# Performance work log

Hardware: AMD Instinct MI355X
Metric: run time of the kernel (lower is better)

The kernel has to match this reference:

```python
import jax, jax.numpy as jnp
import numpy as np

EPS = 1e-12
N_HEADS = 16


def _ln(x, g, b, eps=EPS):
    m = jnp.mean(x, axis=-1, keepdims=True)
    v = jnp.var(x, axis=-1, keepdims=True)
    return (x - m) * jax.lax.rsqrt(v + eps) * g + b


def setup_inputs() -> dict:
    key = jax.random.key(0)
    ks = jax.random.split(key, 8)
    B, S, D, I = 2, 2048, 1024, 4096
    s = 0.02
    f32 = jnp.float32
    return {
        "x": jax.random.normal(ks[0], (B, S, D), f32),
        "input_mask": jnp.zeros((B, 1, 1, S), f32),  # additive mask, 0 = no masking
        "norm_w": jnp.ones((D,), f32),
        "norm_b": jnp.zeros((D,), f32),
        "attn_qkvw": jax.random.normal(ks[1], (D, 3 * D), f32) * s,
        "attn_qkvb": jnp.zeros((3 * D,), f32),
        "attn_ow": jax.random.normal(ks[2], (D, D), f32) * s,
        "attn_ob": jnp.zeros((D,), f32),
        "attn_nw": jnp.ones((D,), f32),
        "attn_nb": jnp.zeros((D,), f32),
        "inter_w": jax.random.normal(ks[3], (D, I), f32) * s,
        "inter_b": jnp.zeros((I,), f32),
        "inter_w1": jax.random.normal(ks[4], (D, I), f32) * s,
        "output_w": jax.random.normal(ks[5], (I, D), f32) * s,
        "output_b": jnp.zeros((D,), f32),
    }


def reference(x, input_mask, norm_w, norm_b, attn_qkvw, attn_qkvb, attn_ow,
              attn_ob, attn_nw, attn_nb, inter_w, inter_b, inter_w1,
              output_w, output_b):
    B, S, D = x.shape
    hd = D // N_HEADS

    # --- fused qkv_gemm: pre-layernorm + QKV GEMM + bias ---
    ln1 = _ln(x, norm_w, norm_b)
    qkv = ln1 @ attn_qkvw + attn_qkvb            # [B,S,3D]
    q, k, v = jnp.split(qkv, 3, axis=-1)

    def to_heads(t):  # [B,S,D] -> [B,H,S,hd]
        return t.reshape(B, S, N_HEADS, hd).transpose(0, 2, 1, 3)

    q, k, v = to_heads(q), to_heads(k), to_heads(v)

    # --- softmax-context attention (scale_attention=True -> 1/sqrt(head_dim)) ---
    scores = jnp.einsum('bhqd,bhkd->bhqk', q, k) / jnp.sqrt(jnp.float32(hd))
    scores = scores + input_mask                 # additive mask [B,1,1,S]
    probs = jax.nn.softmax(scores, axis=-1)
    ctx = jnp.einsum('bhqk,bhkd->bhqd', probs, v)
    ctx = ctx.transpose(0, 2, 1, 3).reshape(B, S, D)

    attn_out = ctx @ attn_ow                     # vector_matmul (no bias)

    # --- fused mlp_gemm: bias+residual add, layernorm, GEMM+bias+gelu ---
    residual_add = attn_out + attn_ob + x
    ln2 = _ln(residual_add, attn_nw, attn_nb)
    intermediate = jax.nn.gelu(ln2 @ inter_w + inter_b, approximate=False)
    # gated path: vector_matmul(mlp input, inter_w1) * intermediate (per source)
    intermediate = (attn_out @ inter_w1) * intermediate

    # --- output projection + bias_residual ---
    out = intermediate @ output_w + output_b + residual_add
    return out
```

## Files before the change

kernel.cpp:

```cpp
#include <hip/hip_runtime.h>
#include <hip/hip_bf16.h>

#define BATCH 2
#define SEQ   2048
#define DIM   1024
#define IDIM  4096
#define NH    16
#define HD    64
#define TOK   (BATCH * SEQ)

typedef __hip_bfloat16 bf16;

typedef short bf16x8_t __attribute__((ext_vector_type(8)));
typedef float f32x4_t  __attribute__((ext_vector_type(4)));

__device__ __forceinline__ float ldv(const float* p, size_t i) { return p[i]; }
__device__ __forceinline__ float ldv(const bf16*  p, size_t i) { return __bfloat162float(p[i]); }
__device__ __forceinline__ void  stv(float* p, size_t i, float v) { p[i] = v; }
__device__ __forceinline__ void  stv(bf16*  p, size_t i, float v) { p[i] = __float2bfloat16(v); }

__device__ __forceinline__ f32x4_t mfma16(bf16x8_t a, bf16x8_t b, f32x4_t c) {
    return __builtin_amdgcn_mfma_f32_16x16x32_bf16(a, b, c, 0, 0, 0);
}

__device__ __forceinline__ void gload16(const bf16* g, bf16* l) {
    __builtin_amdgcn_global_load_lds(
        (const __attribute__((address_space(1))) void*)g,
        (__attribute__((address_space(3))) void*)l, 16, 0, 0);
}

__global__ __launch_bounds__(256) void ln_kernel(const float* __restrict__ in,
                                                 const float* __restrict__ w,
                                                 const float* __restrict__ b,
                                                 bf16* __restrict__ out) {
    const int row = blockIdx.x;
    const int tid = threadIdx.x;
    const float* xr = in + (size_t)row * DIM;

    float v[4], sum = 0.f, sq = 0.f;
#pragma unroll
    for (int i = 0; i < 4; i++) {
        float t = xr[tid + i * 256];
        v[i] = t; sum += t; sq += t * t;
    }
#pragma unroll
    for (int off = 32; off >= 1; off >>= 1) {
        sum += __shfl_xor(sum, off);
        sq  += __shfl_xor(sq,  off);
    }
    __shared__ float s1[4], s2[4];
    int wid = tid >> 6;
    if ((tid & 63) == 0) { s1[wid] = sum; s2[wid] = sq; }
    __syncthreads();
    sum = s1[0] + s1[1] + s1[2] + s1[3];
    sq  = s2[0] + s2[1] + s2[2] + s2[3];

    const float mean = sum * (1.f / DIM);
    const float var  = fmaxf(sq * (1.f / DIM) - mean * mean, 0.f);
    const float rstd = rsqrtf(var + 1e-12f);

    bf16* orow = out + (size_t)row * DIM;
#pragma unroll
    for (int i = 0; i < 4; i++) {
        int idx = tid + i * 256;
        orow[idx] = __float2bfloat16((v[i] - mean) * rstd * w[idx] + b[idx]);
    }
}

__global__ __launch_bounds__(256) void wconv_kernel(const float* __restrict__ W,
                                                    bf16* __restrict__ Wt,
                                                    int K, int N) {
    __shared__ float tile[32][33];
    const int tid = threadIdx.x;
    const int n0 = blockIdx.x * 32;
    const int k0 = blockIdx.y * 32;
    const int c = tid & 31;
    const int r = tid >> 5;
#pragma unroll
    for (int i = 0; i < 4; i++)
        tile[r + i * 8][c] = W[(size_t)(k0 + r + i * 8) * N + n0 + c];
    __syncthreads();
#pragma unroll
    for (int i = 0; i < 4; i++)
        Wt[(size_t)(n0 + r + i * 8) * K + k0 + c] = __float2bfloat16(tile[c][r + i * 8]);
}

#define GBK 32

template<typename TX, int MODE, int TM, int TN>
__global__ __launch_bounds__(256) void mgemm_kernel(const bf16* __restrict__ A,
                                                    const bf16* __restrict__ Bt,
                                                    const float* __restrict__ bias,
                                                    const TX* __restrict__ aux,
                                                    TX* __restrict__ C,
                                                    const float* __restrict__ bias2,
                                                    const float* __restrict__ xin,
                                                    float* __restrict__ C2,
                                                    int M, int N, int K) {
    constexpr int TILE_M = TM * 32;
    constexpr int TILE_N = TN * 32;
    __shared__ alignas(16) bf16 As[TILE_M][GBK];
    __shared__ alignas(16) bf16 Bs[TILE_N][GBK];

    const int tid  = threadIdx.x;
    const int w    = tid >> 6;
    const int lane = tid & 63;
    const int cl   = lane & 15;
    const int qd   = lane >> 4;
    const int wm   = w >> 1;
    const int wn   = w & 1;

    const int gn   = gridDim.x;
    const int lin  = blockIdx.y * gn + blockIdx.x;
    const int span = 8 * gn;
    const int panel = lin / span;
    const int rem   = lin - panel * span;
    const int by    = panel * 8 + (rem & 7);
    const int bx    = rem >> 3;

    const int row0 = by * TILE_M;
    const int col0 = bx * TILE_N;

    const int lrow = lane >> 2;
    const int lkg  = lane & 3;

    f32x4_t acc[TM][TN];
#pragma unroll
    for (int m = 0; m < TM; m++)
#pragma unroll
        for (int n = 0; n < TN; n++) acc[m][n] = {0.f, 0.f, 0.f, 0.f};

    for (int k0 = 0; k0 < K; k0 += GBK) {
        __syncthreads();
#pragma unroll
        for (int i = 0; i < TM / 2; i++) {
            const int r16 = (w * (TM / 2) + i) * 16;
            gload16(A + (size_t)(row0 + r16 + lrow) * K + k0 + lkg * 8, &As[r16][0]);
        }
#pragma unroll
        for (int j = 0; j < TN / 2; j++) {
            const int r16 = (w * (TN / 2) + j) * 16;
            gload16(Bt + (size_t)(col0 + r16 + lrow) * K + k0 + lkg * 8, &Bs[r16][0]);
        }
        __syncthreads();

        bf16x8_t af[TM], bfr[TN];
#pragma unroll
        for (int m = 0; m < TM; m++)
            af[m] = *(const bf16x8_t*)&As[wm * (TM * 16) + m * 16 + cl][qd * 8];
#pragma unroll
        for (int n = 0; n < TN; n++)
            bfr[n] = *(const bf16x8_t*)&Bs[wn * (TN * 16) + n * 16 + cl][qd * 8];
#pragma unroll
        for (int m = 0; m < TM; m++)
#pragma unroll
            for (int n = 0; n < TN; n++)
                acc[m][n] = mfma16(af[m], bfr[n], acc[m][n]);
    }

#pragma unroll
    for (int m = 0; m < TM; m++) {
#pragma unroll
        for (int n = 0; n < TN; n++) {
            const int gc = col0 + wn * (TN * 16) + n * 16 + cl;
            const float bv = (MODE != 2 && MODE != 4 && bias) ? bias[gc] : 0.f;
#pragma unroll
            for (int r = 0; r < 4; r++) {
                const int gr = row0 + wm * (TM * 16) + m * 16 + qd * 4 + r;
                float c = acc[m][n][r] + bv;
                if (MODE == 1) {
                    c = 0.5f * c * (1.f + erff(c * 0.70710678118654752f));
                } else if (MODE == 2) {
                    c *= ldv(aux, (size_t)gr * N + gc);
                } else if (MODE == 3) {
                    c += ldv(aux, (size_t)gr * N + gc);
                }
                stv(C, (size_t)gr * N + gc, c);
                if (MODE == 4) {
                    C2[(size_t)gr * N + gc] = c + bias2[gc] + xin[(size_t)gr * N + gc];
                }
            }
        }
    }
}

#define KCH 64
#define LDP 72
#define NCH (SEQ / KCH)

__global__ __launch_bounds__(256) void attn_mfma_kernel(const bf16* __restrict__ qkv,
                                                        const float* __restrict__ mask,
                                                        bf16* __restrict__ ctx) {
    __shared__ alignas(16) bf16 Klds[KCH][LDP];
    __shared__ alignas(16) bf16 Vtlds[HD][LDP];
    __shared__ alignas(16) bf16 P2[4][4][4][4][16];

    const int tid  = threadIdx.x;
    const int w    = tid >> 6;
    const int lane = tid & 63;
    const int cl   = lane & 15;
    const int qd   = lane >> 4;

    const int qtile = blockIdx.x;
    const int bh    = blockIdx.y;
    const int bb    = bh >> 4;
    const int h     = bh & 15;

    const bf16*  base = qkv + (size_t)bb * SEQ * (3 * DIM) + h * HD;
    const float* mrow = mask + (size_t)bb * SEQ;

    const bf16* qrow = base + (size_t)(qtile * 64 + w * 16 + cl) * (3 * DIM);
    const bf16x8_t aq0 = *(const bf16x8_t*)(qrow + qd * 8);
    const bf16x8_t aq1 = *(const bf16x8_t*)(qrow + 32 + qd * 8);

    const bf16x8_t onesv = {0x3F80, 0x3F80, 0x3F80, 0x3F80,
                            0x3F80, 0x3F80, 0x3F80, 0x3F80};

    const int krow0 = tid >> 3;
    const int kcol  = (tid & 7) * 8;

    bf16x8_t kx[2], vx[2];
    float    mvx[4];
#pragma unroll
    for (int i = 0; i < 2; i++)
        kx[i] = *(const bf16x8_t*)(base + (size_t)(krow0 + i * 32) * (3 * DIM) + DIM + kcol);
#pragma unroll
    for (int p = 0; p < 2; p++)
        vx[p] = *(const bf16x8_t*)(base + (size_t)lane * (3 * DIM) + 2 * DIM + (w + p * 4) * 8);
#pragma unroll
    for (int ks = 0; ks < 4; ks++) mvx[ks] = mrow[ks * 16 + cl];

    f32x4_t O[4] = {{0,0,0,0},{0,0,0,0},{0,0,0,0},{0,0,0,0}};
    float li[4] = {0.f, 0.f, 0.f, 0.f};

    for (int c = 0; c < NCH; c++) {
        __syncthreads();

#pragma unroll
        for (int i = 0; i < 2; i++)
            *(bf16x8_t*)&Klds[krow0 + i * 32][kcol] = kx[i];
#pragma unroll
        for (int p = 0; p < 2; p++) {
            const int dg = w + p * 4;
#pragma unroll
            for (int j = 0; j < 8; j++)
                ((short*)&Vtlds[dg * 8 + j][0])[lane] = vx[p][j];
        }
        float mv[4];
#pragma unroll
        for (int ks = 0; ks < 4; ks++) mv[ks] = mvx[ks];
        __syncthreads();

        if (c + 1 < NCH) {
            const int k0n = (c + 1) * KCH;
#pragma unroll
            for (int i = 0; i < 2; i++)
                kx[i] = *(const bf16x8_t*)(base + (size_t)(k0n + krow0 + i * 32) * (3 * DIM) + DIM + kcol);
#pragma unroll
            for (int p = 0; p < 2; p++)
                vx[p] = *(const bf16x8_t*)(base + (size_t)(k0n + lane) * (3 * DIM) + 2 * DIM + (w + p * 4) * 8);
#pragma unroll
            for (int ks = 0; ks < 4; ks++) mvx[ks] = mrow[k0n + ks * 16 + cl];
        }

        f32x4_t S[4];
#pragma unroll
        for (int ks = 0; ks < 4; ks++) {
            int key = ks * 16 + cl;
            bf16x8_t b0 = *(const bf16x8_t*)&Klds[key][qd * 8];
            bf16x8_t b1 = *(const bf16x8_t*)&Klds[key][32 + qd * 8];
            f32x4_t s2 = {0.f, 0.f, 0.f, 0.f};
            s2 = mfma16(aq0, b0, s2);
            s2 = mfma16(aq1, b1, s2);
            S[ks] = s2;
        }

#pragma unroll
        for (int ks = 0; ks < 4; ks++)
#pragma unroll
            for (int r = 0; r < 4; r++)
                S[ks][r] = __expf(S[ks][r] * 0.125f + mv[ks]);

#pragma unroll
        for (int ks = 0; ks < 4; ks++)
#pragma unroll
            for (int r = 0; r < 4; r++)
                P2[w][ks][r][qd][cl] = __float2bfloat16(S[ks][r]);

        bf16x8_t pa0 = *(const bf16x8_t*)&P2[w][qd >> 1][cl & 3][cl >> 2][(qd & 1) * 8];
        bf16x8_t pa1 = *(const bf16x8_t*)&P2[w][2 + (qd >> 1)][cl & 3][cl >> 2][(qd & 1) * 8];

        f32x4_t lsum = {0.f, 0.f, 0.f, 0.f};
        lsum = mfma16(pa0, onesv, lsum);
        lsum = mfma16(pa1, onesv, lsum);
#pragma unroll
        for (int r = 0; r < 4; r++) li[r] += lsum[r];

#pragma unroll
        for (int ns = 0; ns < 4; ns++) {
            bf16x8_t v0 = *(const bf16x8_t*)&Vtlds[ns * 16 + cl][qd * 8];
            bf16x8_t v1 = *(const bf16x8_t*)&Vtlds[ns * 16 + cl][32 + qd * 8];
            O[ns] = mfma16(pa0, v0, O[ns]);
            O[ns] = mfma16(pa1, v1, O[ns]);
        }
    }

#pragma unroll
    for (int r = 0; r < 4; r++) {
        int row = qtile * 64 + w * 16 + qd * 4 + r;
        bf16* orow = ctx + (size_t)(bb * SEQ + row) * DIM + h * HD;
        float inv = 1.f / li[r];
#pragma unroll
        for (int ns = 0; ns < 4; ns++)
            orow[ns * 16 + cl] = __float2bfloat16(O[ns][r] * inv);
    }
}

extern "C" void kernel_launch(void* const* d_in, const int* in_sizes, int n_in,
                              void* d_out, int out_size, void* d_ws, size_t ws_size,
                              hipStream_t stream) {
    const float* x        = (const float*)d_in[0];
    const float* mask     = (const float*)d_in[1];
    const float* norm_w   = (const float*)d_in[2];
    const float* norm_b   = (const float*)d_in[3];
    const float* qkvw     = (const float*)d_in[4];
    const float* qkvb     = (const float*)d_in[5];
    const float* attn_ow  = (const float*)d_in[6];
    const float* attn_ob  = (const float*)d_in[7];
    const float* attn_nw  = (const float*)d_in[8];
    const float* attn_nb  = (const float*)d_in[9];
    const float* inter_w  = (const float*)d_in[10];
    const float* inter_b  = (const float*)d_in[11];
    const float* inter_w1 = (const float*)d_in[12];
    const float* output_w = (const float*)d_in[13];
    const float* output_b = (const float*)d_in[14];

    float* out = (float*)d_out;
    bf16*  ws  = (bf16*)d_ws;

    const size_t M1 = 1024 * 1024;
    bf16* ln_s      = ws;
    bf16* qkv       = ws + 4 * M1;
    bf16* inter     = ws + 4 * M1;
    bf16* qkvw_t    = ws + 16 * M1;
    bf16* attn_owt  = ws + 19 * M1;
    bf16* attn_out  = ws + 20 * M1;
    bf16* inter_wt  = ws + 24 * M1;
    bf16* inter_w1t = ws + 28 * M1;
    bf16* output_wt = ws + 32 * M1;
    float* resid    = out;

    dim3 blk(256);

    wconv_kernel<<<dim3(3072 / 32, 1024 / 32), blk, 0, stream>>>(qkvw,     qkvw_t,    1024, 3072);
    wconv_kernel<<<dim3(1024 / 32, 1024 / 32), blk, 0, stream>>>(attn_ow,  attn_owt,  1024, 1024);
    wconv_kernel<<<dim3(4096 / 32, 1024 / 32), blk, 0, stream>>>(inter_w,  inter_wt,  1024, 4096);
    wconv_kernel<<<dim3(4096 / 32, 1024 / 32), blk, 0, stream>>>(inter_w1, inter_w1t, 1024, 4096);
    wconv_kernel<<<dim3(1024 / 32, 4096 / 32), blk, 0, stream>>>(output_w, output_wt, 4096, 1024);

    ln_kernel<<<TOK, blk, 0, stream>>>(x, norm_w, norm_b, ln_s);

    mgemm_kernel<bf16, 0, 4, 4><<<dim3(3072 / 128, TOK / 128), blk, 0, stream>>>(
        ln_s, qkvw_t, qkvb, (const bf16*)nullptr, qkv,
        nullptr, nullptr, nullptr, TOK, 3 * DIM, DIM);

    attn_mfma_kernel<<<dim3(SEQ / 64, BATCH * NH), blk, 0, stream>>>(qkv, mask, ln_s);

    mgemm_kernel<bf16, 4, 4, 2><<<dim3(DIM / 64, TOK / 128), blk, 0, stream>>>(
        ln_s, attn_owt, (const float*)nullptr, (const bf16*)nullptr, attn_out,
        attn_ob, x, resid, TOK, DIM, DIM);

    ln_kernel<<<TOK, blk, 0, stream>>>(resid, attn_nw, attn_nb, ln_s);

    mgemm_kernel<bf16, 1, 4, 4><<<dim3(IDIM / 128, TOK / 128), blk, 0, stream>>>(
        ln_s, inter_wt, inter_b, (const bf16*)nullptr, inter,
        nullptr, nullptr, nullptr, TOK, IDIM, DIM);

    mgemm_kernel<bf16, 2, 4, 4><<<dim3(IDIM / 128, TOK / 128), blk, 0, stream>>>(
        attn_out, inter_w1t, (const float*)nullptr, inter, inter,
        nullptr, nullptr, nullptr, TOK, IDIM, DIM);

    mgemm_kernel<float, 3, 4, 2><<<dim3(DIM / 64, TOK / 128), blk, 0, stream>>>(
        inter, output_wt, output_b, resid, out,
        nullptr, nullptr, nullptr, TOK, DIM, IDIM);
}
```

Baseline: 502.8 us.

## Restructure attention with pre-transposed V, double-buffered async LDS loads, permlane P

Adds a separate kernel that transposes V into a head-major [bh][d][seq] buffer so the attention kernel can load V tiles directly. The attention kernel now handles 128 queries per block (two 16-row tiles per wave), double-buffers K/V in XOR-swizzled LDS filled via gload16 with one barrier per chunk, and rearranges the probability fragments with permlane swaps instead of an LDS round trip. This cuts LDS traffic and synchronisation and reuses K/V fragments across two query tiles. In exchange it adds an extra launch and a global V write/read, and the higher register pressure may limit occupancy. The vt buffer shares workspace with attn_out, which is only written after attention finishes.

```diff
diff --git a/kernel.cpp b/kernel.cpp
--- a/kernel.cpp
+++ b/kernel.cpp
@@ -184,22 +184,58 @@
     }
 }
 
+__global__ __launch_bounds__(256) void vtrans_kernel(const bf16* __restrict__ qkv,
+                                                     bf16* __restrict__ vt) {
+    __shared__ bf16 t[64][72];
+    const int tid = threadIdx.x;
+    const int s0  = blockIdx.x * 64;
+    const int bh  = blockIdx.y;
+    const int bb  = bh >> 4;
+    const int h   = bh & 15;
+    const bf16* src = qkv + (size_t)bb * SEQ * (3 * DIM) + 2 * DIM + h * HD;
+    const int r  = tid >> 3;
+    const int cc = tid & 7;
+#pragma unroll
+    for (int i = 0; i < 2; i++)
+        *(bf16x8_t*)&t[r + i * 32][cc * 8] =
+            *(const bf16x8_t*)(src + (size_t)(s0 + r + i * 32) * (3 * DIM) + cc * 8);
+    __syncthreads();
+    bf16* dst = vt + (size_t)bh * HD * SEQ + s0;
+#pragma unroll
+    for (int i = 0; i < 2; i++) {
+        const int d = r + i * 32;
+        bf16x8_t v;
+#pragma unroll
+        for (int j = 0; j < 8; j++)
+            ((short*)&v)[j] = *(const short*)&t[cc * 8 + j][d];
+        *(bf16x8_t*)(dst + (size_t)d * SEQ + cc * 8) = v;
+    }
+}
+
 #define KCH 64
-#define LDP 72
 #define NCH (SEQ / KCH)
 
-__global__ __launch_bounds__(256) void attn_mfma_kernel(const bf16* __restrict__ qkv,
-                                                        const float* __restrict__ mask,
-                                                        bf16* __restrict__ ctx) {
-    __shared__ alignas(16) bf16 Klds[KCH][LDP];
-    __shared__ alignas(16) bf16 Vtlds[HD][LDP];
-    __shared__ alignas(16) bf16 P2[4][4][4][4][16];
+__device__ __forceinline__ unsigned pk2(float lo, float hi) {
+    unsigned a = (unsigned)__bfloat16_as_ushort(__float2bfloat16(lo));
+    unsigned b = (unsigned)__bfloat16_as_ushort(__float2bfloat16(hi));
+    return a | (b << 16);
+}
+
+union PAU { bf16x8_t v; unsigned u[4]; };
+
+__global__ __launch_bounds__(256, 2) void attn_mfma_kernel(const bf16* __restrict__ qkv,
+                                                           const bf16* __restrict__ vt,
+                                                           const float* __restrict__ mask,
+                                                           bf16* __restrict__ ctx) {
+    __shared__ alignas(16) bf16 Kl[2][KCH][64];
+    __shared__ alignas(16) bf16 Vl[2][KCH][64];
 
     const int tid  = threadIdx.x;
     const int w    = tid >> 6;
     const int lane = tid & 63;
     const int cl   = lane & 15;
     const int qd   = lane >> 4;
+    const int c7   = cl & 7;
 
     const int qtile = blockIdx.x;
     const int bh    = blockIdx.y;
@@ -207,112 +243,129 @@
     const int h     = bh & 15;
 
     const bf16*  base = qkv + (size_t)bb * SEQ * (3 * DIM) + h * HD;
+    const bf16*  gK   = base + DIM;
+    const bf16*  gV   = vt + (size_t)bh * HD * SEQ;
     const float* mrow = mask + (size_t)bb * SEQ;
 
-    const bf16* qrow = base + (size_t)(qtile * 64 + w * 16 + cl) * (3 * DIM);
-    const bf16x8_t aq0 = *(const bf16x8_t*)(qrow + qd * 8);
-    const bf16x8_t aq1 = *(const bf16x8_t*)(qrow + 32 + qd * 8);
+    bf16x8_t aq[2][2];
+#pragma unroll
+    for (int qt = 0; qt < 2; qt++) {
+        const bf16* qrow = base + (size_t)(qtile * 128 + w * 32 + qt * 16 + cl) * (3 * DIM);
+        aq[qt][0] = *(const bf16x8_t*)(qrow + qd * 8);
+        aq[qt][1] = *(const bf16x8_t*)(qrow + 32 + qd * 8);
+    }
 
     const bf16x8_t onesv = {0x3F80, 0x3F80, 0x3F80, 0x3F80,
                             0x3F80, 0x3F80, 0x3F80, 0x3F80};
 
-    const int krow0 = tid >> 3;
-    const int kcol  = (tid & 7) * 8;
-
-    bf16x8_t kx[2], vx[2];
-    float    mvx[4];
-#pragma unroll
-    for (int i = 0; i < 2; i++)
-        kx[i] = *(const bf16x8_t*)(base + (size_t)(krow0 + i * 32) * (3 * DIM) + DIM + kcol);
-#pragma unroll
-    for (int p = 0; p < 2; p++)
-        vx[p] = *(const bf16x8_t*)(base + (size_t)lane * (3 * DIM) + 2 * DIM + (w + p * 4) * 8);
-#pragma unroll
-    for (int ks = 0; ks < 4; ks++) mvx[ks] = mrow[ks * 16 + cl];
-
-    f32x4_t O[4] = {{0,0,0,0},{0,0,0,0},{0,0,0,0},{0,0,0,0}};
-    float li[4] = {0.f, 0.f, 0.f, 0.f};
+    const int sr  = lane >> 3;
+    const int scw = (lane & 7) ^ sr;
+
+#pragma unroll
+    for (int i = 0; i < 2; i++) {
+        const int row = i * 32 + w * 8 + sr;
+        gload16(gK + (size_t)row * (3 * DIM) + scw * 8, &Kl[0][i * 32 + w * 8][0]);
+        gload16(gV + (size_t)row * SEQ + scw * 8, &Vl[0][i * 32 + w * 8][0]);
+    }
+    f32x4_t mkx[4];
+#pragma unroll
+    for (int ks = 0; ks < 4; ks++)
+        mkx[ks] = *(const f32x4_t*)&mrow[ks * 16 + qd * 4];
+
+    f32x4_t O[2][4];
+#pragma unroll
+    for (int qt = 0; qt < 2; qt++)
+#pragma unroll
+        for (int ns = 0; ns < 4; ns++) O[qt][ns] = {0.f, 0.f, 0.f, 0.f};
+    f32x4_t li[2] = {{0.f,0.f,0.f,0.f},{0.f,0.f,0.f,0.f}};
 
     for (int c = 0; c < NCH; c++) {
         __syncthreads();
-
-#pragma unroll
-        for (int i = 0; i < 2; i++)
-            *(bf16x8_t*)&Klds[krow0 + i * 32][kcol] = kx[i];
-#pragma unroll
-        for (int p = 0; p < 2; p++) {
-            const int dg = w + p * 4;
-#pragma unroll
-            for (int j = 0; j < 8; j++)
-                ((short*)&Vtlds[dg * 8 + j][0])[lane] = vx[p][j];
-        }
-        float mv[4];
-#pragma unroll
-        for (int ks = 0; ks < 4; ks++) mv[ks] = mvx[ks];
-        __syncthreads();
+        const bf16 (*Kb)[64] = Kl[c & 1];
+        const bf16 (*Vb)[64] = Vl[c & 1];
+
+        f32x4_t mk[4];
+#pragma unroll
+        for (int ks = 0; ks < 4; ks++) mk[ks] = mkx[ks];
 
         if (c + 1 < NCH) {
+            bf16 (*Kn)[64] = Kl[(c + 1) & 1];
+            bf16 (*Vn)[64] = Vl[(c + 1) & 1];
             const int k0n = (c + 1) * KCH;
 #pragma unroll
-            for (int i = 0; i < 2; i++)
-                kx[i] = *(const bf16x8_t*)(base + (size_t)(k0n + krow0 + i * 32) * (3 * DIM) + DIM + kcol);
-#pragma unroll
-            for (int p = 0; p < 2; p++)
-                vx[p] = *(const bf16x8_t*)(base + (size_t)(k0n + lane) * (3 * DIM) + 2 * DIM + (w + p * 4) * 8);
-#pragma unroll
-            for (int ks = 0; ks < 4; ks++) mvx[ks] = mrow[k0n + ks * 16 + cl];
-        }
-
-        f32x4_t S[4];
+            for (int i = 0; i < 2; i++) {
+                const int row = i * 32 + w * 8 + sr;
+                gload16(gK + (size_t)(k0n + row) * (3 * DIM) + scw * 8, &Kn[i * 32 + w * 8][0]);
+                gload16(gV + (size_t)row * SEQ + k0n + scw * 8, &Vn[i * 32 + w * 8][0]);
+            }
+#pragma unroll
+            for (int ks = 0; ks < 4; ks++)
+                mkx[ks] = *(const f32x4_t*)&mrow[k0n + ks * 16 + qd * 4];
+        }
+
+        bf16x8_t kf[4][2];
 #pragma unroll
         for (int ks = 0; ks < 4; ks++) {
-            int key = ks * 16 + cl;
-            bf16x8_t b0 = *(const bf16x8_t*)&Klds[key][qd * 8];
-            bf16x8_t b1 = *(const bf16x8_t*)&Klds[key][32 + qd * 8];
-            f32x4_t s2 = {0.f, 0.f, 0.f, 0.f};
-            s2 = mfma16(aq0, b0, s2);
-            s2 = mfma16(aq1, b1, s2);
-            S[ks] = s2;
-        }
-
-#pragma unroll
-        for (int ks = 0; ks < 4; ks++)
-#pragma unroll
-            for (int r = 0; r < 4; r++)
-                S[ks][r] = __expf(S[ks][r] * 0.125f + mv[ks]);
-
-#pragma unroll
-        for (int ks = 0; ks < 4; ks++)
-#pragma unroll
-            for (int r = 0; r < 4; r++)
-                P2[w][ks][r][qd][cl] = __float2bfloat16(S[ks][r]);
-
-        bf16x8_t pa0 = *(const bf16x8_t*)&P2[w][qd >> 1][cl & 3][cl >> 2][(qd & 1) * 8];
-        bf16x8_t pa1 = *(const bf16x8_t*)&P2[w][2 + (qd >> 1)][cl & 3][cl >> 2][(qd & 1) * 8];
-
-        f32x4_t lsum = {0.f, 0.f, 0.f, 0.f};
-        lsum = mfma16(pa0, onesv, lsum);
-        lsum = mfma16(pa1, onesv, lsum);
-#pragma unroll
-        for (int r = 0; r < 4; r++) li[r] += lsum[r];
+            kf[ks][0] = *(const bf16x8_t*)&Kb[ks * 16 + cl][(qd ^ c7) << 3];
+            kf[ks][1] = *(const bf16x8_t*)&Kb[ks * 16 + cl][((4 + qd) ^ c7) << 3];
+        }
+
+        PAU pa[2][2];
+#pragma unroll
+        for (int qt = 0; qt < 2; qt++) {
+            unsigned Dv[4][2];
+#pragma unroll
+            for (int ks = 0; ks < 4; ks++) {
+                f32x4_t s = {0.f, 0.f, 0.f, 0.f};
+                s = mfma16(kf[ks][0], aq[qt][0], s);
+                s = mfma16(kf[ks][1], aq[qt][1], s);
+                const float e0 = __expf(s[0] * 0.125f + mk[ks][0]);
+                const float e1 = __expf(s[1] * 0.125f + mk[ks][1]);
+                const float e2 = __expf(s[2] * 0.125f + mk[ks][2]);
+                const float e3 = __expf(s[3] * 0.125f + mk[ks][3]);
+                Dv[ks][0] = pk2(e0, e1);
+                Dv[ks][1] = pk2(e2, e3);
+            }
+#pragma unroll
+            for (int rp = 0; rp < 2; rp++) {
+                auto z0 = __builtin_amdgcn_permlane32_swap(Dv[0][rp], Dv[1][rp], false, false);
+                auto w0 = __builtin_amdgcn_permlane16_swap(z0[0], z0[1], false, false);
+                pa[qt][0].u[rp]     = w0[0];
+                pa[qt][0].u[rp + 2] = w0[1];
+                auto z1 = __builtin_amdgcn_permlane32_swap(Dv[2][rp], Dv[3][rp], false, false);
+                auto w1 = __builtin_amdgcn_permlane16_swap(z1[0], z1[1], false, false);
+                pa[qt][1].u[rp]     = w1[0];
+                pa[qt][1].u[rp + 2] = w1[1];
+            }
+            f32x4_t ls = {0.f, 0.f, 0.f, 0.f};
+            ls = mfma16(pa[qt][0].v, onesv, ls);
+            ls = mfma16(pa[qt][1].v, onesv, ls);
+            li[qt] += ls;
+        }
 
 #pragma unroll
         for (int ns = 0; ns < 4; ns++) {
-            bf16x8_t v0 = *(const bf16x8_t*)&Vtlds[ns * 16 + cl][qd * 8];
-            bf16x8_t v1 = *(const bf16x8_t*)&Vtlds[ns * 16 + cl][32 + qd * 8];
-            O[ns] = mfma16(pa0, v0, O[ns]);
-            O[ns] = mfma16(pa1, v1, O[ns]);
-        }
-    }
-
-#pragma unroll
-    for (int r = 0; r < 4; r++) {
-        int row = qtile * 64 + w * 16 + qd * 4 + r;
-        bf16* orow = ctx + (size_t)(bb * SEQ + row) * DIM + h * HD;
-        float inv = 1.f / li[r];
-#pragma unroll
-        for (int ns = 0; ns < 4; ns++)
-            orow[ns * 16 + cl] = __float2bfloat16(O[ns][r] * inv);
+            bf16x8_t v0 = *(const bf16x8_t*)&Vb[ns * 16 + cl][(qd ^ c7) << 3];
+            bf16x8_t v1 = *(const bf16x8_t*)&Vb[ns * 16 + cl][((4 + qd) ^ c7) << 3];
+#pragma unroll
+            for (int qt = 0; qt < 2; qt++) {
+                O[qt][ns] = mfma16(pa[qt][0].v, v0, O[qt][ns]);
+                O[qt][ns] = mfma16(pa[qt][1].v, v1, O[qt][ns]);
+            }
+        }
+    }
+
+#pragma unroll
+    for (int qt = 0; qt < 2; qt++) {
+#pragma unroll
+        for (int r = 0; r < 4; r++) {
+            const int row = qtile * 128 + w * 32 + qt * 16 + qd * 4 + r;
+            bf16* orow = ctx + (size_t)(bb * SEQ + row) * DIM + h * HD;
+            const float inv = 1.f / li[qt][r];
+#pragma unroll
+            for (int ns = 0; ns < 4; ns++)
+                orow[ns * 16 + cl] = __float2bfloat16(O[qt][ns][r] * inv);
+        }
     }
 }
 
@@ -344,6 +397,7 @@
     bf16* inter     = ws + 4 * M1;
     bf16* qkvw_t    = ws + 16 * M1;
     bf16* attn_owt  = ws + 19 * M1;
+    bf16* vt        = ws + 20 * M1;
     bf16* attn_out  = ws + 20 * M1;
     bf16* inter_wt  = ws + 24 * M1;
     bf16* inter_w1t = ws + 28 * M1;
@@ -364,7 +418,9 @@
         ln_s, qkvw_t, qkvb, (const bf16*)nullptr, qkv,
         nullptr, nullptr, nullptr, TOK, 3 * DIM, DIM);
 
-    attn_mfma_kernel<<<dim3(SEQ / 64, BATCH * NH), blk, 0, stream>>>(qkv, mask, ln_s);
+    vtrans_kernel<<<dim3(SEQ / 64, BATCH * NH), blk, 0, stream>>>(qkv, vt);
+
+    attn_mfma_kernel<<<dim3(SEQ / 128, BATCH * NH), blk, 0, stream>>>(qkv, vt, mask, ln_s);
 
     mgemm_kernel<bf16, 4, 4, 2><<<dim3(DIM / 64, TOK / 128), blk, 0, stream>>>(
         ln_s, attn_owt, (const float*)nullptr, (const bf16*)nullptr, attn_out,
```

Result: no change. 499.6 us (-0.6%).
